# Optimization experiments

Hardware: AMD Instinct MI355X
Metric: run time of the kernel (lower is better)

The kernel has to match this reference:

```python
import jax, jax.numpy as jnp
import numpy as np

N_LEVELS = 16
N_FEATS = 2
LOG2_T = 19
TABLE_SIZE = 1 << LOG2_T
BASE_RES = 16
FINEST_RES = 512
DIM = 3
N_POINTS = 2_000_000
PRIMES = jnp.array([1, 2654435761, 805459861], dtype=jnp.uint32)


def _hash_encode(x01, tables, resolutions):
    """Multi-resolution hash grid encoding with trilinear interpolation.
    x01: [N, D] in [0, 1]; tables: [L, T, F]; resolutions: [L] float.
    Returns [N, L*F]."""
    N, D = x01.shape
    T = tables.shape[1]
    # all 2^D corner offsets of the enclosing voxel, shape [2^D, D]
    offsets = jnp.array([[(i >> d) & 1 for d in range(D)] for i in range(1 << D)],
                        dtype=jnp.float32)

    def per_level(table, res):
        pos = x01 * res                      # [N, D]
        p0 = jnp.floor(pos)
        w = pos - p0                         # fractional part, [N, D]
        corners = p0[None, :, :] + offsets[:, None, :]      # [2^D, N, D]
        ci = corners.astype(jnp.uint32)
        hp = ci * PRIMES[None, None, :D]                    # uint32 wraps mod 2^32
        h = hp[..., 0]
        for d in range(1, D):
            h = h ^ hp[..., d]
        idx = (h & jnp.uint32(T - 1)).astype(jnp.int32)     # [2^D, N]
        feats = table[idx]                                  # gather, [2^D, N, F]
        # trilinear weights: prod_d (w_d if corner bit set else 1-w_d)
        wc = jnp.prod(jnp.where(offsets[:, None, :] > 0, w[None], 1.0 - w[None]),
                      axis=-1)                              # [2^D, N]
        return jnp.sum(wc[..., None] * feats, axis=0)       # [N, F]

    f = jax.vmap(per_level)(tables, resolutions)            # [L, N, F]
    return jnp.transpose(f, (1, 0, 2)).reshape(N, -1)       # [N, L*F]


def setup_inputs() -> dict:
    key = jax.random.key(0)
    ks = jax.random.split(key, 8)
    x = jax.random.uniform(ks[0], (N_POINTS, DIM), jnp.float32, -1.0, 1.0)
    tables = jax.random.uniform(ks[1], (N_LEVELS, TABLE_SIZE, N_FEATS),
                                jnp.float32, -1e-4, 1e-4)
    b = np.exp((np.log(FINEST_RES) - np.log(BASE_RES)) / (N_LEVELS - 1))
    resolutions = jnp.asarray(np.floor(BASE_RES * b ** np.arange(N_LEVELS)),
                              dtype=jnp.float32)
    in_dim = N_LEVELS * N_FEATS  # 32
    W1 = jax.random.normal(ks[2], (in_dim, 64), jnp.float32) * (1.0 / np.sqrt(in_dim))
    b1 = jnp.zeros((64,), jnp.float32)
    W2 = jax.random.normal(ks[3], (64, 64), jnp.float32) * (1.0 / 8.0)
    b2 = jnp.zeros((64,), jnp.float32)
    W3 = jax.random.normal(ks[4], (64, 1), jnp.float32) * (1.0 / 8.0)
    b3 = jnp.zeros((1,), jnp.float32)
    return {"x": x, "tables": tables, "resolutions": resolutions,
            "W1": W1, "b1": b1, "W2": W2, "b2": b2, "W3": W3, "b3": b3}


def reference(x, tables, resolutions, W1, b1, W2, b2, W3, b3):
    x01 = x / 2.0 + 0.5                       # map [-1,1] -> [0,1]
    a = _hash_encode(x01, tables, resolutions)  # [N, 32]
    h = jax.nn.relu(a @ W1 + b1)
    h = jax.nn.relu(h @ W2 + b2)
    return h @ W3 + b3                        # [N, 1]
```

## Files before the change

kernel.cpp:

```cpp
#include <hip/hip_runtime.h>
#include <hip/hip_bf16.h>
#include <stdint.h>

#define N_LEVELS   16
#define LOG2_T     19
#define TABLE_SIZE (1u << LOG2_T)
#define PRIME_Y    2654435761u
#define PRIME_Z    805459861u

#define NB        32768
#define SORT_B    256
#define SORT_T    512
#define CVT_B     2048

typedef float v4f __attribute__((ext_vector_type(4)));
typedef _Float16 v8h __attribute__((ext_vector_type(8)));

__device__ __forceinline__ uint32_t part1by2(uint32_t v) {
    v &= 0x3FFu;
    v = (v | (v << 16)) & 0x030000FFu;
    v = (v | (v <<  8)) & 0x0300F00Fu;
    v = (v | (v <<  4)) & 0x030C30C3u;
    v = (v | (v <<  2)) & 0x09249249u;
    return v;
}
__device__ __forceinline__ uint32_t morton_key(float xr, float yr, float zr) {
    int vx = (int)((xr * 0.5f + 0.5f) * 32.0f);
    int vy = (int)((yr * 0.5f + 0.5f) * 32.0f);
    int vz = (int)((zr * 0.5f + 0.5f) * 32.0f);
    vx = vx < 0 ? 0 : (vx > 31 ? 31 : vx);
    vy = vy < 0 ? 0 : (vy > 31 ? 31 : vy);
    vz = vz < 0 ? 0 : (vz > 31 ? 31 : vz);
    return part1by2((uint32_t)vx) | (part1by2((uint32_t)vy) << 1)
         | (part1by2((uint32_t)vz) << 2);
}

__global__ __launch_bounds__(SORT_T)
void hist_cvt_kernel(const float* __restrict__ x, uint32_t* __restrict__ g_hist,
                     int n, int chunk,
                     const float* __restrict__ tables,
                     uint32_t* __restrict__ tab16)
{
    __shared__ uint32_t pack[NB / 2];
    if (blockIdx.x >= SORT_B) {
        const int cb = blockIdx.x - SORT_B;
        const size_t base_pair = (size_t)cb * SORT_T * 4;
        #pragma unroll
        for (int k = 0; k < 4; ++k) {
            const size_t e2 = base_pair + (size_t)k * SORT_T + threadIdx.x;
            const size_t base = e2 * 2;
            const float4 v = *(const float4*)(tables + base * 2);
            union { _Float16 h[2]; uint32_t u; } p0, p1;
            p0.h[0] = (_Float16)v.x; p0.h[1] = (_Float16)v.y;
            p1.h[0] = (_Float16)v.z; p1.h[1] = (_Float16)v.w;
            *(uint2*)(tab16 + base) = make_uint2(p0.u, p1.u);
        }
        return;
    }
    const int b = blockIdx.x, t = threadIdx.x;
    for (int w = t; w < NB / 2; w += SORT_T) pack[w] = 0;
    __syncthreads();
    const int beg = b * chunk;
    const int end = (beg + chunk < n) ? (beg + chunk) : n;
    for (int i = beg + t; i < end; i += SORT_T) {
        const uint32_t key = morton_key(x[3*i], x[3*i+1], x[3*i+2]);
        atomicAdd(&pack[key >> 1], 1u << ((key & 1u) << 4));
    }
    __syncthreads();
    uint32_t* __restrict__ dst = g_hist + (size_t)b * NB;
    for (int w = t; w < NB / 2; w += SORT_T) {
        const uint32_t p = pack[w];
        dst[2*w]     = p & 0xFFFFu;
        dst[2*w + 1] = p >> 16;
    }
}

__global__ __launch_bounds__(256)
void scan_cols_kernel(const uint32_t* __restrict__ g_hist,
                      uint32_t* __restrict__ g_part,
                      uint32_t* __restrict__ totals)
{
    const int key = blockIdx.x * 256 + threadIdx.x;
    uint32_t run = 0;
    #pragma unroll 8
    for (int b = 0; b < SORT_B; ++b) {
        const size_t idx = (size_t)b * NB + key;
        const uint32_t v = g_hist[idx];
        g_part[idx] = run;
        run += v;
    }
    totals[key] = run;
}

__global__ void scan_block_kernel(const uint32_t* __restrict__ counts,
                                  uint32_t* __restrict__ prefix,
                                  uint32_t* __restrict__ blocksum) {
    __shared__ uint32_t s[256];
    const int t = threadIdx.x;
    const int i = blockIdx.x * 256 + t;
    const uint32_t v = counts[i];
    s[t] = v; __syncthreads();
    #pragma unroll
    for (int d = 1; d < 256; d <<= 1) {
        const uint32_t u = (t >= d) ? s[t - d] : 0;
        __syncthreads();
        s[t] += u;
        __syncthreads();
    }
    prefix[i] = s[t] - v;
    if (t == 255) blocksum[blockIdx.x] = s[255];
}

__global__ void scan_top_kernel(const uint32_t* __restrict__ blocksum,
                                uint32_t* __restrict__ blockbase, int nb) {
    __shared__ uint32_t s[1024];
    const int t = threadIdx.x;
    const uint32_t v = (t < nb) ? blocksum[t] : 0;
    s[t] = v; __syncthreads();
    #pragma unroll
    for (int d = 1; d < 1024; d <<= 1) {
        const uint32_t u = (t >= d) ? s[t - d] : 0;
        __syncthreads();
        s[t] += u;
        __syncthreads();
    }
    if (t < nb) blockbase[t] = s[t] - v;
}

__global__ __launch_bounds__(SORT_T)
void scatter_kernel(const float* __restrict__ x,
                    const uint32_t* __restrict__ pref,
                    const uint32_t* __restrict__ bbase,
                    const uint32_t* __restrict__ g_part,
                    float4* __restrict__ xs4,
                    int* __restrict__ perm,
                    int n, int chunk)
{
    __shared__ uint32_t pack[NB / 2];
    const int b = blockIdx.x, t = threadIdx.x;
    for (int w = t; w < NB / 2; w += SORT_T) pack[w] = 0;
    __syncthreads();
    const uint32_t* __restrict__ part = g_part + (size_t)b * NB;
    const int beg = b * chunk;
    const int end = (beg + chunk < n) ? (beg + chunk) : n;
    for (int i = beg + t; i < end; i += SORT_T) {
        const float a = x[3*i], c = x[3*i+1], d = x[3*i+2];
        const uint32_t key = morton_key(a, c, d);
        const uint32_t sh = (key & 1u) << 4;
        uint32_t r = atomicAdd(&pack[key >> 1], 1u << sh);
        r = (r >> sh) & 0xFFFFu;
        const uint32_t pos = pref[key] + bbase[key >> 8] + part[key] + r;
        xs4[pos]  = make_float4(a, c, d, 0.0f);
        perm[pos] = i;
    }
}

__device__ __forceinline__ float2 unpk16(uint32_t u) {
    union { uint32_t u; _Float16 h[2]; } c; c.u = u;
    return make_float2((float)c.h[0], (float)c.h[1]);
}

__global__ __launch_bounds__(256, 8)
void encode_f16_kernel(const float4* __restrict__ xs4,
                       const uint32_t* __restrict__ tab16,
                       const float* __restrict__ resolutions,
                       uint32_t* __restrict__ a_ws2,
                       int n)
{
    const int l = blockIdx.y;
    int p = blockIdx.x * blockDim.x + threadIdx.x;
    if (p >= n) p = n - 1;

    const float4 xv = xs4[p];
    const float x0 = xv.x * 0.5f + 0.5f;
    const float x1 = xv.y * 0.5f + 0.5f;
    const float x2 = xv.z * 0.5f + 0.5f;

    const float res = resolutions[l];
    const float px = x0 * res, py = x1 * res, pz = x2 * res;
    const float fx = floorf(px), fy = floorf(py), fz = floorf(pz);
    const float wx = px - fx, wy = py - fy, wz = pz - fz;
    const uint32_t cx = (uint32_t)fx;
    const uint32_t cy = (uint32_t)fy;
    const uint32_t cz = (uint32_t)fz;

    const uint32_t hy0 = cy * PRIME_Y, hy1 = hy0 + PRIME_Y;
    const uint32_t hz0 = cz * PRIME_Z, hz1 = hz0 + PRIME_Z;

    const float wx0 = 1.0f - wx, wy0 = 1.0f - wy, wz0 = 1.0f - wz;

    const uint32_t* __restrict__ tab = tab16 + (size_t)l * (size_t)TABLE_SIZE;

    const uint32_t hyz[4] = { hy0 ^ hz0, hy1 ^ hz0, hy0 ^ hz1, hy1 ^ hz1 };

    float2 cva[4], cvb[4];

    if ((cx & 1u) == 0u) {
        #pragma unroll
        for (int q = 0; q < 4; ++q) {
            const uint32_t idx_a = (cx ^ hyz[q]) & (TABLE_SIZE - 1u);
            const uint32_t base  = idx_a & ~1u;
            const uint2 u2 = *(const uint2*)(tab + base);
            const float2 lo = unpk16(u2.x), hi2 = unpk16(u2.y);
            const bool hi = (idx_a & 1u) != 0u;
            cva[q] = hi ? hi2 : lo;
            cvb[q] = hi ? lo : hi2;
        }
    } else {
        const uint32_t hx0 = cx, hx1 = cx + 1u;
        #pragma unroll
        for (int q = 0; q < 4; ++q) {
            const uint32_t idx_a = (hx0 ^ hyz[q]) & (TABLE_SIZE - 1u);
            const uint32_t idx_b = (hx1 ^ hyz[q]) & (TABLE_SIZE - 1u);
            cva[q] = unpk16(tab[idx_a]);
            cvb[q] = unpk16(tab[idx_b]);
        }
    }

    float f0 = 0.0f, f1 = 0.0f;
    #pragma unroll
    for (int q = 0; q < 4; ++q) {
        const float yf = (q & 1) ? wy : wy0;
        const float zf = (q & 2) ? wz : wz0;
        const float wgt_a = (wx0 * yf) * zf;
        const float wgt_b = (wx  * yf) * zf;
        f0 = fmaf(wgt_a, cva[q].x, f0);
        f1 = fmaf(wgt_a, cva[q].y, f1);
        f0 = fmaf(wgt_b, cvb[q].x, f0);
        f1 = fmaf(wgt_b, cvb[q].y, f1);
    }

    union { _Float16 h[2]; uint32_t u; } pk;
    pk.h[0] = (_Float16)(f0 * 256.0f);
    pk.h[1] = (_Float16)(f1 * 256.0f);
    __builtin_nontemporal_store(pk.u, a_ws2 + (size_t)l * n + p);
}

__global__ __launch_bounds__(256, 8)
void encode_kernel(const float4* __restrict__ xs4,
                   const float* __restrict__ tables,
                   const float* __restrict__ resolutions,
                   uint32_t* __restrict__ a_ws2,
                   int n)
{
    const int l = blockIdx.y;
    int p = blockIdx.x * blockDim.x + threadIdx.x;
    if (p >= n) p = n - 1;

    const float4 xv = xs4[p];
    const float x0 = xv.x * 0.5f + 0.5f;
    const float x1 = xv.y * 0.5f + 0.5f;
    const float x2 = xv.z * 0.5f + 0.5f;

    const float res = resolutions[l];
    const float px = x0 * res, py = x1 * res, pz = x2 * res;
    const float fx = floorf(px), fy = floorf(py), fz = floorf(pz);
    const float wx = px - fx, wy = py - fy, wz = pz - fz;
    const uint32_t cx = (uint32_t)fx;
    const uint32_t cy = (uint32_t)fy;
    const uint32_t cz = (uint32_t)fz;

    const uint32_t hy0 = cy * PRIME_Y, hy1 = hy0 + PRIME_Y;
    const uint32_t hz0 = cz * PRIME_Z, hz1 = hz0 + PRIME_Z;

    const float wx0 = 1.0f - wx, wy0 = 1.0f - wy, wz0 = 1.0f - wz;

    const float* __restrict__ tab = tables + (size_t)l * (size_t)TABLE_SIZE * 2u;

    const uint32_t hyz[4] = { hy0 ^ hz0, hy1 ^ hz0, hy0 ^ hz1, hy1 ^ hz1 };

    float2 cva[4], cvb[4];

    if ((cx & 1u) == 0u) {
        #pragma unroll
        for (int q = 0; q < 4; ++q) {
            const uint32_t idx_a = (cx ^ hyz[q]) & (TABLE_SIZE - 1u);
            const uint32_t base  = idx_a & ~1u;
            const float4 f4 = *(const float4*)(tab + 2u * base);
            const bool hi = (idx_a & 1u) != 0u;
            cva[q] = hi ? make_float2(f4.z, f4.w) : make_float2(f4.x, f4.y);
            cvb[q] = hi ? make_float2(f4.x, f4.y) : make_float2(f4.z, f4.w);
        }
    } else {
        const uint32_t hx0 = cx, hx1 = cx + 1u;
        #pragma unroll
        for (int q = 0; q < 4; ++q) {
            const uint32_t idx_a = (hx0 ^ hyz[q]) & (TABLE_SIZE - 1u);
            const uint32_t idx_b = (hx1 ^ hyz[q]) & (TABLE_SIZE - 1u);
            cva[q] = *(const float2*)(tab + 2u * idx_a);
            cvb[q] = *(const float2*)(tab + 2u * idx_b);
        }
    }

    float f0 = 0.0f, f1 = 0.0f;
    #pragma unroll
    for (int q = 0; q < 4; ++q) {
        const float yf = (q & 1) ? wy : wy0;
        const float zf = (q & 2) ? wz : wz0;
        const float wgt_a = (wx0 * yf) * zf;
        const float wgt_b = (wx  * yf) * zf;
        f0 = fmaf(wgt_a, cva[q].x, f0);
        f1 = fmaf(wgt_a, cva[q].y, f1);
        f0 = fmaf(wgt_b, cvb[q].x, f0);
        f1 = fmaf(wgt_b, cvb[q].y, f1);
    }

    union { _Float16 h[2]; uint32_t u; } pk;
    pk.h[0] = (_Float16)(f0 * 256.0f);
    pk.h[1] = (_Float16)(f1 * 256.0f);
    __builtin_nontemporal_store(pk.u, a_ws2 + (size_t)l * n + p);
}

#define MLP_CB1 4096
#define MLP_CB2 4160
#define MLP_CW3 4224
__global__ __launch_bounds__(256, 2)
void mlp_mfma_kernel(const uint32_t* __restrict__ a_ws2,
                     const float* __restrict__ W1,
                     const float* __restrict__ b1,
                     const float* __restrict__ W2,
                     const float* __restrict__ b2,
                     const float* __restrict__ W3,
                     const float* __restrict__ b3,
                     const int* __restrict__ perm,
                     float* __restrict__ out,
                     int n)
{
    __shared__ float lds[4 * 64 * 16 + 192];

    const int lane    = threadIdx.x & 63;
    const int wave_id = threadIdx.x >> 6;
    const int m       = lane & 15;
    const int q       = lane >> 4;
    float* __restrict__ myl = &lds[wave_id * 1024];

    if (threadIdx.x < 64) {
        lds[MLP_CB1 + threadIdx.x] = 256.0f * b1[threadIdx.x];
        lds[MLP_CB2 + threadIdx.x] = 256.0f * b2[threadIdx.x];
        lds[MLP_CW3 + threadIdx.x] = W3[threadIdx.x];
    }

    const float b3s = b3[0];

    v8h a1[4];
    #pragma unroll
    for (int t = 0; t < 4; ++t)
        #pragma unroll
        for (int j = 0; j < 8; ++j)
            a1[t][j] = (_Float16)W1[(8 * q + j) * 64 + 16 * t + m];

    v8h a2[2][4];
    #pragma unroll
    for (int c = 0; c < 2; ++c)
        #pragma unroll
        for (int t = 0; t < 4; ++t)
            #pragma unroll
            for (int j = 0; j < 8; ++j)
                a2[c][t][j] = (_Float16)W2[(32 * c + 8 * q + j) * 64 + 16 * t + m];

    __syncthreads();

    const int nt = (n + 15) >> 4;
    const int stride = gridDim.x * 4;
    const int gw = blockIdx.x * 4 + wave_id;
    if (gw >= nt) return;

    union BF { uint32_t w[4]; v8h h; };

    v8h bh;
    {
        const int p0 = gw * 16;
        const int pr = (p0 + m < n) ? (p0 + m) : (n - 1);
        BF ub;
        #pragma unroll
        for (int lv = 0; lv < 4; ++lv)
            ub.w[lv] = __builtin_nontemporal_load(
                a_ws2 + (size_t)(4 * q + lv) * n + pr);
        bh = ub.h;
    }

    for (int tile = gw; tile < nt; tile += stride) {
        const int p0 = tile * 16;

        v8h bhn = bh;
        const int nx = tile + stride;
        if (nx < nt) {
            const int p0n = nx * 16;
            const int prn = (p0n + m < n) ? (p0n + m) : (n - 1);
            BF ub;
            #pragma unroll
            for (int lv = 0; lv < 4; ++lv)
                ub.w[lv] = __builtin_nontemporal_load(
                    a_ws2 + (size_t)(4 * q + lv) * n + prn);
            bhn = ub.h;
        }

        v4f acc1[4];
        #pragma unroll
        for (int t = 0; t < 4; ++t) {
            acc1[t] = *(const v4f*)&lds[MLP_CB1 + 16 * t + 4 * q];
            acc1[t] = __builtin_amdgcn_mfma_f32_16x16x32_f16(a1[t], bh, acc1[t], 0, 0, 0);
        }

        #pragma unroll
        for (int t = 0; t < 4; ++t)
            #pragma unroll
            for (int r = 0; r < 4; ++r)
                myl[(16 * t + 4 * q + r) * 16 + m] = fmaxf(acc1[t][r], 0.0f);
        __threadfence_block();

        v8h b2h[2];
        #pragma unroll
        for (int c = 0; c < 2; ++c)
            #pragma unroll
            for (int j = 0; j < 8; ++j)
                b2h[c][j] = (_Float16)myl[(32 * c + 8 * q + j) * 16 + m];

        v4f acc2[4];
        #pragma unroll
        for (int t = 0; t < 4; ++t) {
            acc2[t] = *(const v4f*)&lds[MLP_CB2 + 16 * t + 4 * q];
            acc2[t] = __builtin_amdgcn_mfma_f32_16x16x32_f16(a2[0][t], b2h[0], acc2[t], 0, 0, 0);
            acc2[t] = __builtin_amdgcn_mfma_f32_16x16x32_f16(a2[1][t], b2h[1], acc2[t], 0, 0, 0);
        }

        float partial = 0.0f;
        #pragma unroll
        for (int t = 0; t < 4; ++t) {
            const v4f w3q = *(const v4f*)&lds[MLP_CW3 + 16 * t + 4 * q];
            #pragma unroll
            for (int r = 0; r < 4; ++r)
                partial = fmaf(fmaxf(acc2[t][r], 0.0f), w3q[r], partial);
        }

        partial += __shfl_xor(partial, 16);
        partial += __shfl_xor(partial, 32);

        if (q == 0 && p0 + m < n)
            out[perm[p0 + m]] = partial * (1.0f / 256.0f) + b3s;

        bh = bhn;
    }
}

__global__ __launch_bounds__(256, 4)
void hashgrid_mlp_fused(const float* __restrict__ x,
                        const float* __restrict__ tables,
                        const float* __restrict__ resolutions,
                        const float* __restrict__ W1,
                        const float* __restrict__ b1,
                        const float* __restrict__ W2,
                        const float* __restrict__ b2,
                        const float* __restrict__ W3,
                        const float* __restrict__ b3,
                        float* __restrict__ out,
                        int n)
{
    const int i  = blockIdx.x * blockDim.x + threadIdx.x;
    const int ip = (i < n) ? i : (n - 1);

    const float x0 = x[3 * ip + 0] * 0.5f + 0.5f;
    const float x1 = x[3 * ip + 1] * 0.5f + 0.5f;
    const float x2 = x[3 * ip + 2] * 0.5f + 0.5f;

    float h1[64];
    #pragma unroll
    for (int j = 0; j < 64; ++j) h1[j] = b1[j];

    #pragma unroll
    for (int l = 0; l < N_LEVELS; ++l) {
        const float res = resolutions[l];
        const float px = x0 * res, py = x1 * res, pz = x2 * res;
        const float fx = floorf(px), fy = floorf(py), fz = floorf(pz);
        const float wx = px - fx, wy = py - fy, wz = pz - fz;
        const uint32_t cx = (uint32_t)fx;
        const uint32_t cy = (uint32_t)fy;
        const uint32_t cz = (uint32_t)fz;
        const uint32_t hx0 = cx,           hx1 = cx + 1u;
        const uint32_t hy0 = cy * PRIME_Y, hy1 = hy0 + PRIME_Y;
        const uint32_t hz0 = cz * PRIME_Z, hz1 = hz0 + PRIME_Z;
        const float wx0 = 1.0f - wx, wy0 = 1.0f - wy, wz0 = 1.0f - wz;
        const float* __restrict__ tab = tables + (size_t)l * (size_t)TABLE_SIZE * 2u;

        float f0 = 0.0f, f1 = 0.0f;
        #pragma unroll
        for (int c = 0; c < 8; ++c) {
            const uint32_t h = ((c & 1) ? hx1 : hx0) ^
                               ((c & 2) ? hy1 : hy0) ^
                               ((c & 4) ? hz1 : hz0);
            const uint32_t idx = h & (TABLE_SIZE - 1u);
            const float2 fv = *(const float2*)(tab + 2u * idx);
            const float wgt = ((c & 1) ? wx : wx0) *
                              ((c & 2) ? wy : wy0) *
                              ((c & 4) ? wz : wz0);
            f0 = fmaf(wgt, fv.x, f0);
            f1 = fmaf(wgt, fv.y, f1);
        }
        const float* __restrict__ w1a = W1 + (2 * l + 0) * 64;
        const float* __restrict__ w1b = W1 + (2 * l + 1) * 64;
        #pragma unroll
        for (int j = 0; j < 64; ++j)
            h1[j] = fmaf(f1, w1b[j], fmaf(f0, w1a[j], h1[j]));
    }

    #pragma unroll
    for (int j = 0; j < 64; ++j) h1[j] = fmaxf(h1[j], 0.0f);

    float accum = b3[0];
    #pragma unroll
    for (int half = 0; half < 2; ++half) {
        float h2[32];
        #pragma unroll
        for (int j = 0; j < 32; ++j) h2[j] = b2[half * 32 + j];
        #pragma unroll
        for (int k = 0; k < 64; ++k) {
            const float hk = h1[k];
            const float* __restrict__ w2row = W2 + k * 64 + half * 32;
            #pragma unroll
            for (int j = 0; j < 32; ++j)
                h2[j] = fmaf(hk, w2row[j], h2[j]);
        }
        #pragma unroll
        for (int j = 0; j < 32; ++j)
            accum = fmaf(fmaxf(h2[j], 0.0f), W3[half * 32 + j], accum);
    }
    out[ip] = accum;
}

extern "C" void kernel_launch(void* const* d_in, const int* in_sizes, int n_in,
                              void* d_out, int out_size, void* d_ws, size_t ws_size,
                              hipStream_t stream) {
    const float* x           = (const float*)d_in[0];
    const float* tables      = (const float*)d_in[1];
    const float* resolutions = (const float*)d_in[2];
    const float* W1          = (const float*)d_in[3];
    const float* b1          = (const float*)d_in[4];
    const float* W2          = (const float*)d_in[5];
    const float* b2          = (const float*)d_in[6];
    const float* W3          = (const float*)d_in[7];
    const float* b3          = (const float*)d_in[8];
    float* out               = (float*)d_out;

    const int n = out_size;
    const int block = 256;
    const int grid_pts = (n + block - 1) / block;
    const int chunk = (n + SORT_B - 1) / SORT_B;

    size_t off = 0;
    #define CARVE(bytes) (off = (off + 255) & ~(size_t)255, off += (bytes), off - (bytes))
    const size_t aws_off   = CARVE((size_t)16 * n * sizeof(uint32_t));
    const size_t xs_off    = CARVE((size_t)n * sizeof(float4));
    const size_t perm_off  = CARVE((size_t)n * sizeof(int));
    const size_t tot_off   = CARVE((size_t)NB * sizeof(uint32_t));
    const size_t pref_off  = CARVE((size_t)NB * sizeof(uint32_t));
    const size_t bsum_off  = CARVE(1024 * sizeof(uint32_t));
    const size_t bbase_off = CARVE(1024 * sizeof(uint32_t));
    const size_t total_ws_B = off;
    const size_t tab16_off = CARVE((size_t)N_LEVELS * TABLE_SIZE * sizeof(uint32_t));
    const size_t total_ws_A = off;
    #undef CARVE

    if (ws_size >= total_ws_B) {
        const bool f16tab = (ws_size >= total_ws_A);
        char* ws = (char*)d_ws;
        uint32_t* a_ws2  = (uint32_t*)(ws + aws_off);
        uint32_t* g_hist = (uint32_t*)(ws + aws_off);
        uint32_t* g_part = (uint32_t*)(ws + aws_off + (size_t)SORT_B * NB * 4);
        float4*   xs4    = (float4*)(ws + xs_off);
        int*      perm   = (int*)(ws + perm_off);
        uint32_t* totals = (uint32_t*)(ws + tot_off);
        uint32_t* pref   = (uint32_t*)(ws + pref_off);
        uint32_t* bsum   = (uint32_t*)(ws + bsum_off);
        uint32_t* bbase  = (uint32_t*)(ws + bbase_off);
        uint32_t* tab16  = (uint32_t*)(ws + tab16_off);

        const int hist_grid = SORT_B + (f16tab ? CVT_B : 0);
        hist_cvt_kernel<<<hist_grid, SORT_T, 0, stream>>>(
            x, g_hist, n, chunk, tables, f16tab ? tab16 : (uint32_t*)nullptr);
        scan_cols_kernel<<<NB / 256, block, 0, stream>>>(g_hist, g_part, totals);
        scan_block_kernel<<<NB / 256, block, 0, stream>>>(totals, pref, bsum);
        scan_top_kernel<<<1, 1024, 0, stream>>>(bsum, bbase, NB / 256);
        scatter_kernel<<<SORT_B, SORT_T, 0, stream>>>(
            x, pref, bbase, g_part, xs4, perm, n, chunk);

        dim3 grid_enc(grid_pts, N_LEVELS);
        if (f16tab) {
            encode_f16_kernel<<<grid_enc, block, 0, stream>>>(
                xs4, tab16, resolutions, a_ws2, n);
        } else {
            encode_kernel<<<grid_enc, block, 0, stream>>>(
                xs4, tables, resolutions, a_ws2, n);
        }
        mlp_mfma_kernel<<<1024, block, 0, stream>>>(a_ws2, W1, b1, W2, b2, W3, b3,
                                                    perm, out, n);
    } else {
        hashgrid_mlp_fused<<<grid_pts, block, 0, stream>>>(
            x, tables, resolutions, W1, b1, W2, b2, W3, b3, out, n);
    }
}
```

Before: 581.3 us.

## Replace stable per-block counting sort with global-atomic histogram and single-kernel scan

Replaces the stable multi-block counting sort (per-block shared histograms, column scan, two-level scan, stable scatter) with global atomic histogram, one 1024-thread scan over 32K bins, and a scatter using global atomicAdd for positions. This drops the large per-block histogram arrays and several launches, at the cost of heavy global atomic contention on 32K bins and a non-deterministic order within each bin. The encode kernels also drop the parity branch and always issue two gathers per corner pair, which simplifies control flow but can add loads.

```diff
diff --git a/kernel.cpp b/kernel.cpp
--- a/kernel.cpp
+++ b/kernel.cpp
@@ -9,9 +9,9 @@
 #define PRIME_Z    805459861u
 
 #define NB        32768
-#define SORT_B    256
-#define SORT_T    512
-#define CVT_B     2048
+#define HIST_B    1024
+#define CVT_B     4096
+#define SCAT_B    2048
 
 typedef float v4f __attribute__((ext_vector_type(4)));
 typedef _Float16 v8h __attribute__((ext_vector_type(8)));
@@ -35,19 +35,18 @@
          | (part1by2((uint32_t)vz) << 2);
 }
 
-__global__ __launch_bounds__(SORT_T)
-void hist_cvt_kernel(const float* __restrict__ x, uint32_t* __restrict__ g_hist,
-                     int n, int chunk,
+__global__ __launch_bounds__(256)
+void hist_cvt_kernel(const float* __restrict__ x, uint32_t* __restrict__ hist,
+                     int n,
                      const float* __restrict__ tables,
                      uint32_t* __restrict__ tab16)
 {
-    __shared__ uint32_t pack[NB / 2];
-    if (blockIdx.x >= SORT_B) {
-        const int cb = blockIdx.x - SORT_B;
-        const size_t base_pair = (size_t)cb * SORT_T * 4;
+    if (blockIdx.x >= HIST_B) {
+        const int cb = blockIdx.x - HIST_B;
+        const size_t base_pair = (size_t)cb * 256 * 4;
         #pragma unroll
         for (int k = 0; k < 4; ++k) {
-            const size_t e2 = base_pair + (size_t)k * SORT_T + threadIdx.x;
+            const size_t e2 = base_pair + (size_t)k * 256 + threadIdx.x;
             const size_t base = e2 * 2;
             const float4 v = *(const float4*)(tables + base * 2);
             union { _Float16 h[2]; uint32_t u; } p0, p1;
@@ -57,66 +56,24 @@
         }
         return;
     }
-    const int b = blockIdx.x, t = threadIdx.x;
-    for (int w = t; w < NB / 2; w += SORT_T) pack[w] = 0;
-    __syncthreads();
-    const int beg = b * chunk;
-    const int end = (beg + chunk < n) ? (beg + chunk) : n;
-    for (int i = beg + t; i < end; i += SORT_T) {
+    const int stride = HIST_B * 256;
+    for (int i = blockIdx.x * 256 + threadIdx.x; i < n; i += stride) {
         const uint32_t key = morton_key(x[3*i], x[3*i+1], x[3*i+2]);
-        atomicAdd(&pack[key >> 1], 1u << ((key & 1u) << 4));
-    }
-    __syncthreads();
-    uint32_t* __restrict__ dst = g_hist + (size_t)b * NB;
-    for (int w = t; w < NB / 2; w += SORT_T) {
-        const uint32_t p = pack[w];
-        dst[2*w]     = p & 0xFFFFu;
-        dst[2*w + 1] = p >> 16;
-    }
-}
-
-__global__ __launch_bounds__(256)
-void scan_cols_kernel(const uint32_t* __restrict__ g_hist,
-                      uint32_t* __restrict__ g_part,
-                      uint32_t* __restrict__ totals)
-{
-    const int key = blockIdx.x * 256 + threadIdx.x;
-    uint32_t run = 0;
-    #pragma unroll 8
-    for (int b = 0; b < SORT_B; ++b) {
-        const size_t idx = (size_t)b * NB + key;
-        const uint32_t v = g_hist[idx];
-        g_part[idx] = run;
-        run += v;
-    }
-    totals[key] = run;
-}
-
-__global__ void scan_block_kernel(const uint32_t* __restrict__ counts,
-                                  uint32_t* __restrict__ prefix,
-                                  uint32_t* __restrict__ blocksum) {
-    __shared__ uint32_t s[256];
-    const int t = threadIdx.x;
-    const int i = blockIdx.x * 256 + t;
-    const uint32_t v = counts[i];
-    s[t] = v; __syncthreads();
-    #pragma unroll
-    for (int d = 1; d < 256; d <<= 1) {
-        const uint32_t u = (t >= d) ? s[t - d] : 0;
-        __syncthreads();
-        s[t] += u;
-        __syncthreads();
-    }
-    prefix[i] = s[t] - v;
-    if (t == 255) blocksum[blockIdx.x] = s[255];
-}
-
-__global__ void scan_top_kernel(const uint32_t* __restrict__ blocksum,
-                                uint32_t* __restrict__ blockbase, int nb) {
+        atomicAdd(&hist[key], 1u);
+    }
+}
+
+__global__ __launch_bounds__(1024)
+void scan32k_kernel(const uint32_t* __restrict__ cnt,
+                    uint32_t* __restrict__ base)
+{
     __shared__ uint32_t s[1024];
     const int t = threadIdx.x;
-    const uint32_t v = (t < nb) ? blocksum[t] : 0;
-    s[t] = v; __syncthreads();
+    uint32_t loc[32];
+    uint32_t sum = 0;
+    #pragma unroll
+    for (int j = 0; j < 32; ++j) { loc[j] = cnt[t * 32 + j]; sum += loc[j]; }
+    s[t] = sum; __syncthreads();
     #pragma unroll
     for (int d = 1; d < 1024; d <<= 1) {
         const uint32_t u = (t >= d) ? s[t - d] : 0;
@@ -124,32 +81,23 @@
         s[t] += u;
         __syncthreads();
     }
-    if (t < nb) blockbase[t] = s[t] - v;
-}
-
-__global__ __launch_bounds__(SORT_T)
+    uint32_t run = s[t] - sum;
+    #pragma unroll
+    for (int j = 0; j < 32; ++j) { base[t * 32 + j] = run; run += loc[j]; }
+}
+
+__global__ __launch_bounds__(256)
 void scatter_kernel(const float* __restrict__ x,
-                    const uint32_t* __restrict__ pref,
-                    const uint32_t* __restrict__ bbase,
-                    const uint32_t* __restrict__ g_part,
+                    uint32_t* __restrict__ base,
                     float4* __restrict__ xs4,
                     int* __restrict__ perm,
-                    int n, int chunk)
-{
-    __shared__ uint32_t pack[NB / 2];
-    const int b = blockIdx.x, t = threadIdx.x;
-    for (int w = t; w < NB / 2; w += SORT_T) pack[w] = 0;
-    __syncthreads();
-    const uint32_t* __restrict__ part = g_part + (size_t)b * NB;
-    const int beg = b * chunk;
-    const int end = (beg + chunk < n) ? (beg + chunk) : n;
-    for (int i = beg + t; i < end; i += SORT_T) {
+                    int n)
+{
+    const int stride = SCAT_B * 256;
+    for (int i = blockIdx.x * 256 + threadIdx.x; i < n; i += stride) {
         const float a = x[3*i], c = x[3*i+1], d = x[3*i+2];
         const uint32_t key = morton_key(a, c, d);
-        const uint32_t sh = (key & 1u) << 4;
-        uint32_t r = atomicAdd(&pack[key >> 1], 1u << sh);
-        r = (r >> sh) & 0xFFFFu;
-        const uint32_t pos = pref[key] + bbase[key >> 8] + part[key] + r;
+        const uint32_t pos = atomicAdd(&base[key], 1u);
         xs4[pos]  = make_float4(a, c, d, 0.0f);
         perm[pos] = i;
     }
@@ -195,26 +143,16 @@
 
     float2 cva[4], cvb[4];
 
-    if ((cx & 1u) == 0u) {
-        #pragma unroll
-        for (int q = 0; q < 4; ++q) {
-            const uint32_t idx_a = (cx ^ hyz[q]) & (TABLE_SIZE - 1u);
-            const uint32_t base  = idx_a & ~1u;
-            const uint2 u2 = *(const uint2*)(tab + base);
-            const float2 lo = unpk16(u2.x), hi2 = unpk16(u2.y);
-            const bool hi = (idx_a & 1u) != 0u;
-            cva[q] = hi ? hi2 : lo;
-            cvb[q] = hi ? lo : hi2;
-        }
-    } else {
-        const uint32_t hx0 = cx, hx1 = cx + 1u;
-        #pragma unroll
-        for (int q = 0; q < 4; ++q) {
-            const uint32_t idx_a = (hx0 ^ hyz[q]) & (TABLE_SIZE - 1u);
-            const uint32_t idx_b = (hx1 ^ hyz[q]) & (TABLE_SIZE - 1u);
-            cva[q] = unpk16(tab[idx_a]);
-            cvb[q] = unpk16(tab[idx_b]);
-        }
+    #pragma unroll
+    for (int q = 0; q < 4; ++q) {
+        const uint32_t idx_a = (cx        ^ hyz[q]) & (TABLE_SIZE - 1u);
+        const uint32_t idx_b = ((cx + 1u) ^ hyz[q]) & (TABLE_SIZE - 1u);
+        const uint2 u2a = *(const uint2*)(tab + (idx_a & ~1u));
+        const uint2 u2b = *(const uint2*)(tab + (idx_b & ~1u));
+        const uint32_t wa = (idx_a & 1u) ? u2a.y : u2a.x;
+        const uint32_t wb = (idx_b & 1u) ? u2b.y : u2b.x;
+        cva[q] = unpk16(wa);
+        cvb[q] = unpk16(wb);
     }
 
     float f0 = 0.0f, f1 = 0.0f;
@@ -269,40 +207,21 @@
 
     const uint32_t hyz[4] = { hy0 ^ hz0, hy1 ^ hz0, hy0 ^ hz1, hy1 ^ hz1 };
 
-    float2 cva[4], cvb[4];
-
-    if ((cx & 1u) == 0u) {
-        #pragma unroll
-        for (int q = 0; q < 4; ++q) {
-            const uint32_t idx_a = (cx ^ hyz[q]) & (TABLE_SIZE - 1u);
-            const uint32_t base  = idx_a & ~1u;
-            const float4 f4 = *(const float4*)(tab + 2u * base);
-            const bool hi = (idx_a & 1u) != 0u;
-            cva[q] = hi ? make_float2(f4.z, f4.w) : make_float2(f4.x, f4.y);
-            cvb[q] = hi ? make_float2(f4.x, f4.y) : make_float2(f4.z, f4.w);
-        }
-    } else {
-        const uint32_t hx0 = cx, hx1 = cx + 1u;
-        #pragma unroll
-        for (int q = 0; q < 4; ++q) {
-            const uint32_t idx_a = (hx0 ^ hyz[q]) & (TABLE_SIZE - 1u);
-            const uint32_t idx_b = (hx1 ^ hyz[q]) & (TABLE_SIZE - 1u);
-            cva[q] = *(const float2*)(tab + 2u * idx_a);
-            cvb[q] = *(const float2*)(tab + 2u * idx_b);
-        }
-    }
-
     float f0 = 0.0f, f1 = 0.0f;
     #pragma unroll
     for (int q = 0; q < 4; ++q) {
+        const uint32_t idx_a = (cx        ^ hyz[q]) & (TABLE_SIZE - 1u);
+        const uint32_t idx_b = ((cx + 1u) ^ hyz[q]) & (TABLE_SIZE - 1u);
+        const float2 fa = *(const float2*)(tab + 2u * idx_a);
+        const float2 fb = *(const float2*)(tab + 2u * idx_b);
         const float yf = (q & 1) ? wy : wy0;
         const float zf = (q & 2) ? wz : wz0;
         const float wgt_a = (wx0 * yf) * zf;
         const float wgt_b = (wx  * yf) * zf;
-        f0 = fmaf(wgt_a, cva[q].x, f0);
-        f1 = fmaf(wgt_a, cva[q].y, f1);
-        f0 = fmaf(wgt_b, cvb[q].x, f0);
-        f1 = fmaf(wgt_b, cvb[q].y, f1);
+        f0 = fmaf(wgt_a, fa.x, f0);
+        f1 = fmaf(wgt_a, fa.y, f1);
+        f0 = fmaf(wgt_b, fb.x, f0);
+        f1 = fmaf(wgt_b, fb.y, f1);
     }
 
     union { _Float16 h[2]; uint32_t u; } pk;
@@ -544,17 +463,14 @@
     const int n = out_size;
     const int block = 256;
     const int grid_pts = (n + block - 1) / block;
-    const int chunk = (n + SORT_B - 1) / SORT_B;
 
     size_t off = 0;
     #define CARVE(bytes) (off = (off + 255) & ~(size_t)255, off += (bytes), off - (bytes))
     const size_t aws_off   = CARVE((size_t)16 * n * sizeof(uint32_t));
     const size_t xs_off    = CARVE((size_t)n * sizeof(float4));
     const size_t perm_off  = CARVE((size_t)n * sizeof(int));
-    const size_t tot_off   = CARVE((size_t)NB * sizeof(uint32_t));
-    const size_t pref_off  = CARVE((size_t)NB * sizeof(uint32_t));
-    const size_t bsum_off  = CARVE(1024 * sizeof(uint32_t));
-    const size_t bbase_off = CARVE(1024 * sizeof(uint32_t));
+    const size_t hist_off  = CARVE((size_t)NB * sizeof(uint32_t));
+    const size_t base_off  = CARVE((size_t)NB * sizeof(uint32_t));
     const size_t total_ws_B = off;
     const size_t tab16_off = CARVE((size_t)N_LEVELS * TABLE_SIZE * sizeof(uint32_t));
     const size_t total_ws_A = off;
@@ -564,24 +480,19 @@
         const bool f16tab = (ws_size >= total_ws_A);
         char* ws = (char*)d_ws;
         uint32_t* a_ws2  = (uint32_t*)(ws + aws_off);
-        uint32_t* g_hist = (uint32_t*)(ws + aws_off);
-        uint32_t* g_part = (uint32_t*)(ws + aws_off + (size_t)SORT_B * NB * 4);
         float4*   xs4    = (float4*)(ws + xs_off);
         int*      perm   = (int*)(ws + perm_off);
-        uint32_t* totals = (uint32_t*)(ws + tot_off);
-        uint32_t* pref   = (uint32_t*)(ws + pref_off);
-        uint32_t* bsum   = (uint32_t*)(ws + bsum_off);
-        uint32_t* bbase  = (uint32_t*)(ws + bbase_off);
+        uint32_t* hist   = (uint32_t*)(ws + hist_off);
+        uint32_t* base   = (uint32_t*)(ws + base_off);
         uint32_t* tab16  = (uint32_t*)(ws + tab16_off);
 
-        const int hist_grid = SORT_B + (f16tab ? CVT_B : 0);
-        hist_cvt_kernel<<<hist_grid, SORT_T, 0, stream>>>(
-            x, g_hist, n, chunk, tables, f16tab ? tab16 : (uint32_t*)nullptr);
-        scan_cols_kernel<<<NB / 256, block, 0, stream>>>(g_hist, g_part, totals);
-        scan_block_kernel<<<NB / 256, block, 0, stream>>>(totals, pref, bsum);
-        scan_top_kernel<<<1, 1024, 0, stream>>>(bsum, bbase, NB / 256);
-        scatter_kernel<<<SORT_B, SORT_T, 0, stream>>>(
-            x, pref, bbase, g_part, xs4, perm, n, chunk);
+        hipMemsetAsync(hist, 0, (size_t)NB * sizeof(uint32_t), stream);
+
+        const int hist_grid = HIST_B + (f16tab ? CVT_B : 0);
+        hist_cvt_kernel<<<hist_grid, block, 0, stream>>>(
+            x, hist, n, tables, f16tab ? tab16 : (uint32_t*)nullptr);
+        scan32k_kernel<<<1, 1024, 0, stream>>>(hist, base);
+        scatter_kernel<<<SCAT_B, block, 0, stream>>>(x, base, xs4, perm, n);
 
         dim3 grid_enc(grid_pts, N_LEVELS);
         if (f16tab) {
```

New measurement: 745.4 us. 28.2% more time.
